# Optimization experiments

Measured on AMD Instinct MI355X. Metric: run time of the kernel, lower is better.

The kernel has to match this reference:

```python
import jax, jax.numpy as jnp
import numpy as np

N_HEAD = 12
D_MODEL = 768
B, T = 1, 1024


def _rope(x):
    # x: (B, H, T, Dh). Matches torch RoPE: split even/odd, cat halves.
    Dh = x.shape[-1]
    t = x.shape[2]
    inv_freq = 1.0 / (10000.0 ** (jnp.arange(0, Dh, 2, dtype=jnp.float32) / Dh))
    freqs = jnp.arange(t, dtype=jnp.float32)[:, None] * inv_freq[None, :]  # (T, Dh/2)
    cos = jnp.cos(freqs)[None, None]  # (1,1,T,Dh/2)
    sin = jnp.sin(freqs)[None, None]
    x1 = x[..., 0::2]
    x2 = x[..., 1::2]
    return jnp.concatenate([-x2 * sin + x1 * cos, x1 * sin + x2 * cos], axis=-1)


def _wedge(x, A, id_bias):
    # S = (A - A^T) + diag(id_bias_h), per head h; x: (B,H,T,Dh)
    skew = A - A.T  # (Dh, Dh)
    S = skew[None, :, :] + jax.vmap(jnp.diag)(id_bias)  # (H, Dh, Dh)
    flow = jnp.einsum('bhtd,hde->bhte', x, S)
    return x + flow


def _forward(x, WV_w, WV_b, WK_w, WK_b, WQ_w, A, id_bias, sink, v_nulls, WO_w, WO_b):
    b, t, c = x.shape
    n_br = WO_w.shape[0]
    n_sh = n_br
    dh = c // n_br
    h_tot = n_br * n_sh
    scale = dh ** -0.5

    q = (x @ WQ_w).reshape(b, t, h_tot, dh).transpose(0, 2, 1, 3)      # (B,Htot,T,Dh)
    k_base = (x @ WK_w + WK_b).reshape(b, t, n_sh, dh).transpose(0, 2, 1, 3)
    v_base = (x @ WV_w + WV_b).reshape(b, t, n_sh, dh).transpose(0, 2, 1, 3)
    k = jnp.tile(k_base, (1, n_br, 1, 1))  # (B,Htot,T,Dh)
    v = jnp.tile(v_base, (1, n_br, 1, 1))

    q = _rope(_wedge(q, A, id_bias))
    k = _rope(_wedge(k, A, id_bias))

    scores = jnp.einsum('bhtd,bhsd->bhts', q, k) * scale  # (B,Htot,T,T)
    causal = jnp.tril(jnp.ones((t, t), dtype=bool))
    scores = jnp.where(causal[None, None], scores, -jnp.inf)

    sinks = jnp.broadcast_to(sink.reshape(1, h_tot, 1, 1), (b, h_tot, t, 1))
    probs = jax.nn.softmax(jnp.concatenate([scores, sinks], axis=-1), axis=-1)
    probs_tok, probs_sink = probs[..., :t], probs[..., t:]

    out_tok = jnp.einsum('bhts,bhsd->bhtd', probs_tok, v)
    out_sink = probs_sink * v_nulls.reshape(h_tot, dh)[None, :, None, :]
    ctx = out_tok + out_sink  # (B,Htot,T,Dh)

    ctx = ctx.reshape(b, n_br, n_sh, t, dh).transpose(0, 1, 3, 2, 4).reshape(b, n_br, t, c)
    y = jnp.einsum('bntc,ncd->bntd', ctx, WO_w) + WO_b[None, :, None, :]
    return y.mean(axis=1)  # (B,T,C)


def setup_inputs() -> dict:
    key = jax.random.key(0)
    ks = jax.random.split(key, 12)
    c = D_MODEL
    n_br = N_HEAD
    dh = c // n_br
    h_tot = n_br * n_br
    s = 0.02
    return {
        'x': jax.random.normal(ks[0], (B, T, c), dtype=jnp.float32),
        'WV_w': jax.random.normal(ks[1], (c, c), dtype=jnp.float32) * s,
        'WV_b': jnp.zeros((c,), dtype=jnp.float32),
        'WK_w': jax.random.normal(ks[2], (c, c), dtype=jnp.float32) * s,
        'WK_b': jnp.zeros((c,), dtype=jnp.float32),
        'WQ_w': jax.random.normal(ks[3], (c, c * n_br), dtype=jnp.float32) * s,
        'A': jax.random.normal(ks[4], (dh, dh), dtype=jnp.float32) * s,
        'id_bias': jax.random.normal(ks[5], (h_tot, dh), dtype=jnp.float32) * s,
        'sink': jax.random.normal(ks[6], (h_tot,), dtype=jnp.float32) * s,
        'v_nulls': jax.random.normal(ks[7], (n_br, c), dtype=jnp.float32) * s,
        'WO_w': jax.random.normal(ks[8], (n_br, c, c), dtype=jnp.float32) * (1.0 / np.sqrt(c)),
        'WO_b': jnp.zeros((n_br, c), dtype=jnp.float32),
    }


def reference(x, WV_w, WV_b, WK_w, WK_b, WQ_w, A, id_bias, sink, v_nulls, WO_w, WO_b):
    return _forward(x, WV_w, WV_b, WK_w, WK_b, WQ_w, A, id_bias, sink, v_nulls, WO_w, WO_b)
```

## Files before the change

kernel.cpp:

```cpp
#include <hip/hip_runtime.h>
#include <hip/hip_bf16.h>

#define T_SEQ   1024
#define C_MODEL 768
#define N_BR    12
#define DH      64
#define H_TOT   144
#define NQ      9216

typedef __bf16 bf16x8 __attribute__((ext_vector_type(8)));
typedef float  f32x4  __attribute__((ext_vector_type(4)));
typedef unsigned short u16;

#define SM_OFF 3.0f

__device__ __forceinline__ void gload16(void* lds, const void* g)
{
    __builtin_amdgcn_global_load_lds(
        (const __attribute__((address_space(1))) void*)g,
        (__attribute__((address_space(3))) void*)lds, 16, 0, 0);
}

__device__ __forceinline__ void split1(float x, u16& h, u16& l)
{
    __bf16 bh = (__bf16)x;
    __bf16 bl = (__bf16)(x - (float)bh);
    h = __builtin_bit_cast(u16, bh);
    l = __builtin_bit_cast(u16, bl);
}

__device__ __forceinline__ u16 tobf(float x)
{
    return __builtin_bit_cast(u16, (__bf16)x);
}

__device__ __forceinline__ int swb(int row, int byteoff)
{
    return row * 128 + (byteoff ^ ((row & 7) << 4));
}

__device__ __forceinline__ bf16x8 ldsr8(const u16* p, int byteoff)
{
    return *reinterpret_cast<const bf16x8*>(reinterpret_cast<const char*>(p) + byteoff);
}

__device__ __forceinline__ void convt_body(const float* __restrict__ W,
                                           u16* __restrict__ out, int K, int N,
                                           int nx, int ky, float (*t)[33], int tid)
{
    const int n0 = nx * 32;
    const int k0 = ky * 32;
    const int tx = tid & 31;
    const int ty = tid >> 5;
    #pragma unroll
    for (int r = 0; r < 4; ++r)
        t[ty + r * 8][tx] = W[(size_t)(k0 + ty + r * 8) * N + n0 + tx];
    __syncthreads();
    #pragma unroll
    for (int r = 0; r < 4; ++r)
        out[(size_t)(n0 + ty + r * 8) * K + k0 + tx] = tobf(t[tx][ty + r * 8]);
}

__global__ __launch_bounds__(256)
void prep_kernel(const float* __restrict__ x, u16* __restrict__ xh,
                 const float* __restrict__ Amat, const float* __restrict__ id_bias,
                 u16* __restrict__ Mth, u16* __restrict__ Mtl,
                 const float* __restrict__ WO_b, float* __restrict__ mbias,
                 float* __restrict__ tab,
                 const float* __restrict__ WO_w, u16* __restrict__ wot,
                 const float* __restrict__ WK_w, const float* __restrict__ WV_w,
                 u16* __restrict__ wkvt)
{
    __shared__ float tsh[32][33];
    const int b   = blockIdx.x;
    const int tid = threadIdx.x;

    if (b < 128) {
        const int idx = b * 256 + tid;
        const int t = idx >> 5, i = idx & 31;
        const float inv = expf(-(float)i * (logf(10000.f) / 32.f));
        const float fr = (float)t * inv;
        tab[t * 64 + i]      = cosf(fr);
        tab[t * 64 + 32 + i] = sinf(fr);
    } else if (b < 272) {
        const int h = b - 128;
        const int base = tid * 16;
        #pragma unroll
        for (int i = 0; i < 16; ++i) {
            const int idx = base + i;
            const int e = idx >> 6, d = idx & 63;
            float v = Amat[d * 64 + e] - Amat[e * 64 + d];
            if (d == e) v += 1.0f + id_bias[h * 64 + d];
            u16 hh, ll;
            split1(v, hh, ll);
            Mth[(size_t)h * 4096 + idx] = hh;
            Mtl[(size_t)h * 4096 + idx] = ll;
        }
    } else if (b < 275) {
        const int d = (b - 272) * 256 + tid;
        if (d < C_MODEL) {
            float s = 0.f;
            #pragma unroll
            for (int n = 0; n < N_BR; ++n) s += WO_b[n * C_MODEL + d];
            mbias[d] = s * (1.0f / 12.0f);
        }
    } else if (b < 1043) {
        const size_t i = (size_t)(b - 275) * 1024 + tid * 4;
        float4 v = *reinterpret_cast<const float4*>(&x[i]);
        ushort4 o = { tobf(v.x), tobf(v.y), tobf(v.z), tobf(v.w) };
        *reinterpret_cast<ushort4*>(&xh[i]) = o;
    } else if (b < 7955) {
        const int u = b - 1043;
        convt_body(WO_w, wot, NQ, C_MODEL, u % 24, u / 24, tsh, tid);
    } else if (b < 8531) {
        const int u = b - 7955;
        convt_body(WK_w, wkvt, C_MODEL, C_MODEL, u % 24, u / 24, tsh, tid);
    } else {
        const int u = b - 8531;
        convt_body(WV_w, wkvt + 589824, C_MODEL, C_MODEL, u % 24, u / 24, tsh, tid);
    }
}

#define BM 128
#define BN 128
#define BK 32

__global__ __launch_bounds__(256)
void gemm_bf16_kernel(const u16* __restrict__ A, const u16* __restrict__ B,
                      float* __restrict__ Cp, int M, int N, int K)
{
    __shared__ __align__(16) u16 sA[BM * BK], sB[BN * BK];

    const int tid  = threadIdx.x;
    const int lane = tid & 63;
    const int wid  = tid >> 6;
    const int m0   = blockIdx.y * BM;
    const int n0   = blockIdx.x * BN;
    const int kc   = K / gridDim.z;
    const int kbeg = blockIdx.z * kc;
    const int kend = kbeg + kc;

    const int wm = (wid >> 1) * 64;
    const int wn = (wid & 1) * 64;

    f32x4 acc[4][4];
    #pragma unroll
    for (int i = 0; i < 4; ++i)
        #pragma unroll
        for (int j = 0; j < 4; ++j)
            #pragma unroll
            for (int r = 0; r < 4; ++r) acc[i][j][r] = 0.f;

    const int r0 = tid >> 2;
    const int c0 = tid & 3;
    const int rA = wm + (lane & 15);
    const int rB = wn + (lane & 15);
    const int co = (lane >> 4) * 8;

    for (int k0 = kbeg; k0 < kend; k0 += BK) {
        gload16(&sA[(size_t)tid * 8],         &A[(size_t)(m0 + r0)      * K + k0 + c0 * 8]);
        gload16(&sA[(size_t)(tid + 256) * 8], &A[(size_t)(m0 + r0 + 64) * K + k0 + c0 * 8]);
        gload16(&sB[(size_t)tid * 8],         &B[(size_t)(n0 + r0)      * K + k0 + c0 * 8]);
        gload16(&sB[(size_t)(tid + 256) * 8], &B[(size_t)(n0 + r0 + 64) * K + k0 + c0 * 8]);
        __syncthreads();

        bf16x8 ah[4], bh[4];
        #pragma unroll
        for (int i = 0; i < 4; ++i)
            ah[i] = *reinterpret_cast<const bf16x8*>(&sA[(size_t)(rA + i * 16) * BK + co]);
        #pragma unroll
        for (int j = 0; j < 4; ++j)
            bh[j] = *reinterpret_cast<const bf16x8*>(&sB[(size_t)(rB + j * 16) * BK + co]);
        #pragma unroll
        for (int i = 0; i < 4; ++i)
            #pragma unroll
            for (int j = 0; j < 4; ++j)
                acc[i][j] = __builtin_amdgcn_mfma_f32_16x16x32_bf16(ah[i], bh[j], acc[i][j], 0, 0, 0);
        __syncthreads();
    }

    float* Cz = Cp + (size_t)blockIdx.z * M * N;
    const int crow0 = m0 + wm + (lane >> 4) * 4;
    const int ccol0 = n0 + wn + (lane & 15);
    #pragma unroll
    for (int i = 0; i < 4; ++i)
        #pragma unroll
        for (int j = 0; j < 4; ++j)
            #pragma unroll
            for (int r = 0; r < 4; ++r)
                Cz[(size_t)(crow0 + i * 16 + r) * N + ccol0 + j * 16] = acc[i][j][r];
}

__global__ __launch_bounds__(256)
void gemm_q_rope_kernel(const u16* __restrict__ A, const u16* __restrict__ B,
                        const float* __restrict__ tab, u16* __restrict__ Q2)
{
    __shared__ __align__(16) u16 sA[BM * BK], sB[BN * BK];

    const int K = C_MODEL;
    const int tid  = threadIdx.x;
    const int lane = tid & 63;
    const int wid  = tid >> 6;
    const int m0   = blockIdx.y * BM;
    const int n0   = blockIdx.x * BN;

    const int wm = (wid >> 1) * 64;
    const int wn = (wid & 1) * 64;
    const int g  = lane >> 4;
    const int li = lane & 15;

    f32x4 acc[4][4];
    #pragma unroll
    for (int i = 0; i < 4; ++i)
        #pragma unroll
        for (int j = 0; j < 4; ++j)
            #pragma unroll
            for (int r = 0; r < 4; ++r) acc[i][j][r] = 0.f;

    const int r0 = tid >> 2;
    const int c0 = tid & 3;
    const int rA = wm + li;
    const int rB = wn + li;
    const int co = g * 8;

    for (int k0 = 0; k0 < K; k0 += BK) {
        gload16(&sA[(size_t)tid * 8],         &A[(size_t)(m0 + r0)      * K + k0 + c0 * 8]);
        gload16(&sA[(size_t)(tid + 256) * 8], &A[(size_t)(m0 + r0 + 64) * K + k0 + c0 * 8]);
        gload16(&sB[(size_t)tid * 8],         &B[(size_t)(n0 + r0)      * K + k0 + c0 * 8]);
        gload16(&sB[(size_t)(tid + 256) * 8], &B[(size_t)(n0 + r0 + 64) * K + k0 + c0 * 8]);
        __syncthreads();

        bf16x8 ah[4], bh[4];
        #pragma unroll
        for (int i = 0; i < 4; ++i)
            ah[i] = *reinterpret_cast<const bf16x8*>(&sA[(size_t)(rA + i * 16) * BK + co]);
        #pragma unroll
        for (int j = 0; j < 4; ++j)
            bh[j] = *reinterpret_cast<const bf16x8*>(&sB[(size_t)(rB + j * 16) * BK + co]);
        #pragma unroll
        for (int i = 0; i < 4; ++i)
            #pragma unroll
            for (int j = 0; j < 4; ++j)
                acc[i][j] = __builtin_amdgcn_mfma_f32_16x16x32_bf16(ah[i], bh[j], acc[i][j], 0, 0, 0);
        __syncthreads();
    }

    const int h  = (n0 + wn) >> 6;
    const bool ev = (li & 1) == 0;
    #pragma unroll
    for (int j = 0; j < 4; ++j) {
        const int e  = j * 16 + li;
        const int i2 = e >> 1;
        #pragma unroll
        for (int i = 0; i < 4; ++i) {
            #pragma unroll
            for (int r = 0; r < 4; ++r) {
                const int t = m0 + wm + i * 16 + g * 4 + r;
                const float own = acc[i][j][r];
                const float oth = __shfl_xor(own, 1);
                const float cs = tab[t * 64 + i2];
                const float sn = tab[t * 64 + 32 + i2];
                float o; int ch;
                if (ev) { o = own * cs - oth * sn; ch = i2; }
                else    { o = oth * sn + own * cs; ch = 32 + i2; }
                Q2[((size_t)h * T_SEQ + t) * 64 + ch] = tobf(o * 0.125f);
            }
        }
    }
}

__global__ __launch_bounds__(256)
void reduce_kernel(const float* __restrict__ part, float* __restrict__ out,
                   const float* __restrict__ bias, int MN, int N, int Z, float alpha)
{
    const int i = (blockIdx.x * 256 + threadIdx.x) * 4;
    if (i >= MN) return;
    float4 s = *reinterpret_cast<const float4*>(&part[i]);
    for (int z = 1; z < Z; ++z) {
        float4 p = *reinterpret_cast<const float4*>(&part[(size_t)z * MN + i]);
        s.x += p.x; s.y += p.y; s.z += p.z; s.w += p.w;
    }
    s.x *= alpha; s.y *= alpha; s.z *= alpha; s.w *= alpha;
    if (bias) {
        const int c = i % N;
        s.x += bias[c]; s.y += bias[c + 1]; s.z += bias[c + 2]; s.w += bias[c + 3];
    }
    *reinterpret_cast<float4*>(&out[i]) = s;
}

__global__ __launch_bounds__(256)
void reduce_kv_kernel(const float* __restrict__ part, float* __restrict__ out,
                      const float* __restrict__ kb, const float* __restrict__ vb,
                      int MN, int Z)
{
    const int i = (blockIdx.x * 256 + threadIdx.x) * 4;
    if (i >= MN) return;
    float4 s = *reinterpret_cast<const float4*>(&part[i]);
    for (int z = 1; z < Z; ++z) {
        float4 p = *reinterpret_cast<const float4*>(&part[(size_t)z * MN + i]);
        s.x += p.x; s.y += p.y; s.z += p.z; s.w += p.w;
    }
    const int c = i % 1536;
    const float* bp = (c < 768) ? (kb + c) : (vb + c - 768);
    s.x += bp[0]; s.y += bp[1]; s.z += bp[2]; s.w += bp[3];
    *reinterpret_cast<float4*>(&out[i]) = s;
}

__global__ __launch_bounds__(256)
void fold_wq_kernel(const float* __restrict__ WQ, const u16* __restrict__ Mth,
                    const u16* __restrict__ Mtl, u16* __restrict__ wqt)
{
    __shared__ __align__(16) u16 sMh[4096], sMl[4096];
    __shared__ __align__(16) u16 sB[8192];

    const int h   = blockIdx.x;
    const int k0  = blockIdx.y * 128;
    const int tid = threadIdx.x;
    const int lane = tid & 63, w = tid >> 6, g = lane >> 4, li = lane & 15;

    {
        const char* gmh = (const char*)(Mth + (size_t)h * 4096);
        const char* gml = (const char*)(Mtl + (size_t)h * 4096);
        #pragma unroll
        for (int p = 0; p < 2; ++p) {
            const int u = p * 256 + tid;
            const int row = u >> 3, off = (u & 7) * 16;
            const int src = swb(row, off);
            gload16((char*)sMh + u * 16, gmh + src);
            gload16((char*)sMl + u * 16, gml + src);
        }
    }
    {
        const int r    = tid >> 1;
        const int half = tid & 1;
        const float* src = WQ + (size_t)(k0 + r) * NQ + h * 64 + half * 32;
        #pragma unroll
        for (int q = 0; q < 8; ++q) {
            float4 v = *reinterpret_cast<const float4*>(&src[q * 4]);
            ushort4 o = { tobf(v.x), tobf(v.y), tobf(v.z), tobf(v.w) };
            const int byte = swb(r, half * 64 + q * 8);
            *reinterpret_cast<ushort4*>(reinterpret_cast<char*>(sB) + byte) = o;
        }
    }
    __syncthreads();

    f32x4 acc[4][2];
    #pragma unroll
    for (int i = 0; i < 4; ++i)
        #pragma unroll
        for (int jj = 0; jj < 2; ++jj)
            #pragma unroll
            for (int r = 0; r < 4; ++r) acc[i][jj][r] = 0.f;

    bf16x8 ah[4][2], al[4][2];
    #pragma unroll
    for (int i = 0; i < 4; ++i)
        #pragma unroll
        for (int ks = 0; ks < 2; ++ks) {
            ah[i][ks] = ldsr8(sMh, swb(16 * i + li, ks * 64 + g * 16));
            al[i][ks] = ldsr8(sMl, swb(16 * i + li, ks * 64 + g * 16));
        }
    #pragma unroll
    for (int jj = 0; jj < 2; ++jj) {
        const int brow = 16 * (2 * w + jj) + li;
        #pragma unroll
        for (int ks = 0; ks < 2; ++ks) {
            bf16x8 bh = ldsr8(sB, swb(brow, ks * 64 + g * 16));
            #pragma unroll
            for (int i = 0; i < 4; ++i) {
                acc[i][jj] = __builtin_amdgcn_mfma_f32_16x16x32_bf16(ah[i][ks], bh, acc[i][jj], 0, 0, 0);
                acc[i][jj] = __builtin_amdgcn_mfma_f32_16x16x32_bf16(al[i][ks], bh, acc[i][jj], 0, 0, 0);
            }
        }
    }

    #pragma unroll
    for (int i = 0; i < 4; ++i)
        #pragma unroll
        for (int jj = 0; jj < 2; ++jj) {
            const int kc = k0 + 16 * (2 * w + jj) + li;
            #pragma unroll
            for (int r = 0; r < 4; ++r) {
                const int e = 16 * i + g * 4 + r;
                wqt[((size_t)h * 64 + e) * 768 + kc] = tobf(acc[i][jj][r]);
            }
        }
}

__global__ __launch_bounds__(256)
void wedge_mfma_kernel(const float* __restrict__ X, u16* __restrict__ Y,
                       const u16* __restrict__ Mth, const u16* __restrict__ Mtl,
                       const float* __restrict__ tab, int inStride, int headMod)
{
    const int h   = blockIdx.x;
    const int t0  = blockIdx.y * 64;
    const int tid = threadIdx.x;
    const int lane = tid & 63;
    const int w    = tid >> 6;
    const int g    = lane >> 4;
    const int li   = lane & 15;

    __shared__ __align__(16) u16 sX[4096], sMh[4096], sMl[4096];

    {
        const int r  = tid >> 2;
        const int c0 = (tid & 3) * 16;
        const float* xrow = X + (size_t)(t0 + r) * inStride + (h % headMod) * 64;
        #pragma unroll
        for (int q = 0; q < 4; ++q) {
            const int c = c0 + q * 4;
            float4 v = *reinterpret_cast<const float4*>(&xrow[c]);
            ushort4 hv = { tobf(v.x), tobf(v.y), tobf(v.z), tobf(v.w) };
            *reinterpret_cast<ushort4*>(reinterpret_cast<char*>(sX) + swb(r, 2 * c)) = hv;
        }
    }
    {
        const char* gmh = (const char*)(Mth + (size_t)h * 4096);
        const char* gml = (const char*)(Mtl + (size_t)h * 4096);
        #pragma unroll
        for (int u = 0; u < 2; ++u) {
            const int L = (u * 256 + tid) * 16;
            const int row = L >> 7, off = L & 127;
            const int src = swb(row, off);
            gload16(reinterpret_cast<char*>(sMh) + L, gmh + src);
            gload16(reinterpret_cast<char*>(sMl) + L, gml + src);
        }
    }
    __syncthreads();

    f32x4 acc[4];
    #pragma unroll
    for (int j = 0; j < 4; ++j)
        #pragma unroll
        for (int r = 0; r < 4; ++r) acc[j][r] = 0.f;

    bf16x8 ah[2];
    #pragma unroll
    for (int ks = 0; ks < 2; ++ks)
        ah[ks] = ldsr8(sX, swb(w * 16 + li, ks * 64 + g * 16));
    #pragma unroll
    for (int ks = 0; ks < 2; ++ks)
        #pragma unroll
        for (int j = 0; j < 4; ++j) {
            bf16x8 bh = ldsr8(sMh, swb(16 * j + li, ks * 64 + g * 16));
            bf16x8 bl = ldsr8(sMl, swb(16 * j + li, ks * 64 + g * 16));
            acc[j] = __builtin_amdgcn_mfma_f32_16x16x32_bf16(ah[ks], bh, acc[j], 0, 0, 0);
            acc[j] = __builtin_amdgcn_mfma_f32_16x16x32_bf16(ah[ks], bl, acc[j], 0, 0, 0);
        }

    const bool ev = (li & 1) == 0;
    #pragma unroll
    for (int j = 0; j < 4; ++j) {
        const int e = 16 * j + li;
        const int i2 = e >> 1;
        #pragma unroll
        for (int r = 0; r < 4; ++r) {
            const int t = t0 + w * 16 + g * 4 + r;
            const float own = acc[j][r];
            const float oth = __shfl_xor(own, 1);
            const float cs = tab[t * 64 + i2];
            const float sn = tab[t * 64 + 32 + i2];
            float o; int ch;
            if (ev) { o = own * cs - oth * sn; ch = i2; }
            else    { o = oth * sn + own * cs; ch = 32 + i2; }
            Y[((size_t)h * T_SEQ + t) * 64 + ch] = tobf(o);
        }
    }
}

__global__ __launch_bounds__(256)
void vt_kernel(const float* __restrict__ vb, u16* __restrict__ Vt, int stride)
{
    __shared__ float Ls[64][65];
    const int s  = blockIdx.x;
    const int t0 = blockIdx.y * 64;
    const int tid = threadIdx.x;
    {
        const int r  = tid >> 2;
        const int c0 = (tid & 3) * 16;
        const float* row = vb + (size_t)(t0 + r) * stride + s * 64;
        #pragma unroll
        for (int q = 0; q < 4; ++q) {
            float4 v = *reinterpret_cast<const float4*>(&row[c0 + q * 4]);
            Ls[r][c0 + q * 4 + 0] = v.x; Ls[r][c0 + q * 4 + 1] = v.y;
            Ls[r][c0 + q * 4 + 2] = v.z; Ls[r][c0 + q * 4 + 3] = v.w;
        }
    }
    __syncthreads();
    {
        const int d  = tid >> 2;
        const int tq = (tid & 3) * 16;
        u16* orow = Vt + ((size_t)s * 64 + d) * T_SEQ + t0 + tq;
        #pragma unroll
        for (int q = 0; q < 4; ++q) {
            ushort4 o;
            o.x = tobf(Ls[tq + q * 4 + 0][d]);
            o.y = tobf(Ls[tq + q * 4 + 1][d]);
            o.z = tobf(Ls[tq + q * 4 + 2][d]);
            o.w = tobf(Ls[tq + q * 4 + 3][d]);
            *reinterpret_cast<ushort4*>(&orow[q * 4]) = o;
        }
    }
}

template<bool DIAG>
__device__ __forceinline__ void attn_tile64(
    int kv0, int rowb, int h, int s, int tid, int w, int g, int li,
    const u16* __restrict__ K2, const u16* __restrict__ Vt,
    u16* sK, u16* sV, u16* sP, const bf16x8* qa,
    f32x4* acc, float* psum)
{
    {
        const char* gk = (const char*)(K2 + ((size_t)h * T_SEQ + kv0) * 64);
        const char* gv = (const char*)Vt + (size_t)s * 131072 + kv0 * 2;
        #pragma unroll
        for (int p = 0; p < 2; ++p) {
            const int u = p * 256 + tid;
            const int row = u >> 3, off = (u & 7) * 16;
            gload16((char*)sK + u * 16, gk + row * 128 + (off ^ ((row & 7) << 4)));
            gload16((char*)sV + u * 16, gv + row * 2048 + (off ^ ((row & 7) << 4)));
        }
    }
    __syncthreads();

    f32x4 sacc[4];
    #pragma unroll
    for (int j = 0; j < 4; ++j)
        #pragma unroll
        for (int r = 0; r < 4; ++r) sacc[j][r] = 0.f;

    __builtin_amdgcn_s_setprio(1);
    #pragma unroll
    for (int ks = 0; ks < 2; ++ks)
        #pragma unroll
        for (int j = 0; j < 4; ++j) {
            bf16x8 kb = ldsr8(sK, swb(16 * j + li, ks * 64 + g * 16));
            sacc[j] = __builtin_amdgcn_mfma_f32_16x16x32_bf16(qa[ks], kb, sacc[j], 0, 0, 0);
        }
    __builtin_amdgcn_s_setprio(0);

    char* pb = (char*)sP + w * 2048;
    #pragma unroll
    for (int j = 0; j < 4; ++j) {
        const int colj = kv0 + 16 * j + li;
        #pragma unroll
        for (int r = 0; r < 4; ++r) {
            float sv_ = sacc[j][r];
            if (DIAG && colj > rowb + r) sv_ = -__builtin_inff();
            const float p = __expf(sv_ - SM_OFF);
            psum[r] += p;
            const int prow = g * 4 + r;
            *reinterpret_cast<u16*>(pb + prow * 128 +
                ((2 * (16 * j + li)) ^ ((prow & 7) << 4))) = tobf(p);
        }
    }

    __builtin_amdgcn_s_setprio(1);
    #pragma unroll
    for (int ks = 0; ks < 2; ++ks) {
        bf16x8 pa = *reinterpret_cast<const bf16x8*>(
            pb + li * 128 + ((ks * 64 + g * 16) ^ ((li & 7) << 4)));
        #pragma unroll
        for (int j = 0; j < 4; ++j) {
            bf16x8 vb = ldsr8(sV, swb(16 * j + li, ks * 64 + g * 16));
            acc[j] = __builtin_amdgcn_mfma_f32_16x16x32_bf16(pa, vb, acc[j], 0, 0, 0);
        }
    }
    __builtin_amdgcn_s_setprio(0);
    __syncthreads();
}

__global__ __launch_bounds__(256)
void attn_mfma_kernel(const u16* __restrict__ Q2, const u16* __restrict__ K2,
                      const u16* __restrict__ Vt, const float* __restrict__ sink,
                      const float* __restrict__ v_nulls, u16* __restrict__ ctxb)
{
    const int h  = blockIdx.x;
    const int qt = 15 - (int)blockIdx.y;
    const int s  = h % N_BR;
    const int tid  = threadIdx.x;
    const int lane = tid & 63, w = tid >> 6, g = lane >> 4, li = lane & 15;

    __shared__ __align__(16) u16 sQ[4096];
    __shared__ __align__(16) u16 sK[4096];
    __shared__ __align__(16) u16 sV[4096];
    __shared__ __align__(16) u16 sP[4096];

    {
        const char* gq = (const char*)(Q2 + ((size_t)h * T_SEQ + qt * 64) * 64);
        #pragma unroll
        for (int p = 0; p < 2; ++p) {
            const int u = p * 256 + tid;
            const int row = u >> 3, off = (u & 7) * 16;
            gload16((char*)sQ + u * 16, gq + row * 128 + (off ^ ((row & 7) << 4)));
        }
    }
    __syncthreads();

    bf16x8 qa[2];
    #pragma unroll
    for (int ks = 0; ks < 2; ++ks)
        qa[ks] = ldsr8(sQ, swb(w * 16 + li, ks * 64 + g * 16));

    f32x4 acc[4];
    #pragma unroll
    for (int j = 0; j < 4; ++j)
        #pragma unroll
        for (int r = 0; r < 4; ++r) acc[j][r] = 0.f;
    float psum[4] = {0.f, 0.f, 0.f, 0.f};

    const int rowb = qt * 64 + w * 16 + g * 4;
    for (int kt = 0; kt < qt; ++kt)
        attn_tile64<false>(kt * 64, rowb, h, s, tid, w, g, li, K2, Vt, sK, sV, sP, qa, acc, psum);
    attn_tile64<true>(qt * 64, rowb, h, s, tid, w, g, li, K2, Vt, sK, sV, sP, qa, acc, psum);

    #pragma unroll
    for (int r = 0; r < 4; ++r)
        #pragma unroll
        for (int d = 8; d >= 1; d >>= 1) psum[r] += __shfl_xor(psum[r], d);

    const float es = __expf(sink[h] - SM_OFF);
    #pragma unroll
    for (int r = 0; r < 4; ++r) {
        const float rz = 1.0f / (psum[r] + es);
        const int trow = qt * 64 + w * 16 + g * 4 + r;
        #pragma unroll
        for (int j = 0; j < 4; ++j) {
            const int col = 16 * j + li;
            const float outv = (acc[j][r] + es * v_nulls[h * 64 + col]) * rz;
            ctxb[(size_t)trow * NQ + h * 64 + col] = tobf(outv);
        }
    }
}

extern "C" void kernel_launch(void* const* d_in, const int* in_sizes, int n_in,
                              void* d_out, int out_size, void* d_ws, size_t ws_size,
                              hipStream_t stream)
{
    (void)in_sizes; (void)n_in; (void)out_size; (void)ws_size;

    const float* x       = (const float*)d_in[0];
    const float* WV_w    = (const float*)d_in[1];
    const float* WV_b    = (const float*)d_in[2];
    const float* WK_w    = (const float*)d_in[3];
    const float* WK_b    = (const float*)d_in[4];
    const float* WQ_w    = (const float*)d_in[5];
    const float* Amat    = (const float*)d_in[6];
    const float* id_bias = (const float*)d_in[7];
    const float* sink    = (const float*)d_in[8];
    const float* v_nulls = (const float*)d_in[9];
    const float* WO_w    = (const float*)d_in[10];
    const float* WO_b    = (const float*)d_in[11];
    float* out = (float*)d_out;

    float* tab    = (float*)d_ws;
    float* mbias  = tab + 65536;
    float* kvbase = mbias + 768;
    u16* Mth  = (u16*)(kvbase + 1572864);
    u16* Mtl  = Mth + 589824;
    u16* xh   = Mtl + 589824;
    u16* wqt  = xh + 786432;
    u16* wkvt = wqt + 7077888;
    u16* wot  = wkvt + 1179648;
    u16* K2   = wot + 7077888;
    u16* Vt   = K2 + 9437184;
    u16* Q2   = Vt + 786432;
    u16* ctxb = Q2 + 9437184;
    float* pkv = (float*)(ctxb + 9437184);

    float* outpart = (float*)K2;

    const dim3 blk(256);

    prep_kernel<<<dim3(9107), blk, 0, stream>>>(
        x, xh, Amat, id_bias, Mth, Mtl, WO_b, mbias, tab, WO_w, wot, WK_w, WV_w, wkvt);

    fold_wq_kernel<<<dim3(H_TOT, 6), blk, 0, stream>>>(WQ_w, Mth, Mtl, wqt);

    gemm_bf16_kernel<<<dim3(12, 8, 4), blk, 0, stream>>>(
        xh, wkvt, pkv, T_SEQ, 1536, C_MODEL);
    reduce_kv_kernel<<<dim3(1536), blk, 0, stream>>>(pkv, kvbase, WK_b, WV_b, 1572864, 4);

    wedge_mfma_kernel<<<dim3(H_TOT, 16), blk, 0, stream>>>(
        kvbase, K2, Mth, Mtl, tab, 1536, N_BR);
    vt_kernel<<<dim3(12, 16), blk, 0, stream>>>(kvbase + 768, Vt, 1536);

    gemm_q_rope_kernel<<<dim3(72, 8), blk, 0, stream>>>(xh, wqt, tab, Q2);

    attn_mfma_kernel<<<dim3(H_TOT, 16), blk, 0, stream>>>(
        Q2, K2, Vt, sink, v_nulls, ctxb);

    gemm_bf16_kernel<<<dim3(6, 8, 12), blk, 0, stream>>>(
        ctxb, wot, outpart, T_SEQ, C_MODEL, NQ);
    reduce_kernel<<<dim3(768), blk, 0, stream>>>(
        outpart, out, mbias, 786432, C_MODEL, 12, 1.0f / 12.0f);
}
```

Before: 191.4 us.

## Double-buffer attention K/V, keep P in registers, shrink GEMM M-tiles

The attention kernel now double-buffers K/V tiles in LDS, prefetching the next tile while computing the current one. It swaps MFMA operand order so the S^T layout lets the probabilities be packed straight into bf16 registers, which removes the shared-memory P round trip and one barrier per tile. The Q-projection and output GEMMs move to 64x128 tiles with twice as many blocks, aiming for better occupancy and wave count. In exchange, LDS use and the index logic grow, and the K rows are permuted on load to match the transposed layout.

```diff
diff --git a/kernel.cpp b/kernel.cpp
--- a/kernel.cpp
+++ b/kernel.cpp
@@ -10,6 +10,7 @@
 
 typedef __bf16 bf16x8 __attribute__((ext_vector_type(8)));
 typedef float  f32x4  __attribute__((ext_vector_type(4)));
+typedef unsigned int u32x4 __attribute__((ext_vector_type(4)));
 typedef unsigned short u16;
 
 #define SM_OFF 3.0f
@@ -32,6 +33,13 @@
 __device__ __forceinline__ u16 tobf(float x)
 {
     return __builtin_bit_cast(u16, (__bf16)x);
+}
+
+__device__ __forceinline__ unsigned cvtpk(float a, float b)
+{
+    unsigned r;
+    asm("v_cvt_pk_bf16_f32 %0, %1, %2" : "=v"(r) : "v"(a), "v"(b));
+    return r;
 }
 
 __device__ __forceinline__ int swb(int row, int byteoff)
@@ -192,53 +200,113 @@
 }
 
 __global__ __launch_bounds__(256)
+void gemm64_kernel(const u16* __restrict__ A, const u16* __restrict__ B,
+                   float* __restrict__ Cp, int M, int N, int K)
+{
+    __shared__ __align__(16) u16 sA[64 * BK], sB[128 * BK];
+
+    const int tid  = threadIdx.x;
+    const int lane = tid & 63;
+    const int wid  = tid >> 6;
+    const int m0   = blockIdx.y * 64;
+    const int n0   = blockIdx.x * 128;
+    const int kc   = K / gridDim.z;
+    const int kbeg = blockIdx.z * kc;
+    const int kend = kbeg + kc;
+
+    const int wm = (wid >> 1) * 32;
+    const int wn = (wid & 1) * 64;
+    const int g  = lane >> 4;
+    const int li = lane & 15;
+
+    f32x4 acc[2][4];
+    #pragma unroll
+    for (int i = 0; i < 2; ++i)
+        #pragma unroll
+        for (int j = 0; j < 4; ++j)
+            #pragma unroll
+            for (int r = 0; r < 4; ++r) acc[i][j][r] = 0.f;
+
+    const int r0 = tid >> 2;
+    const int c0 = (tid & 3) * 8;
+
+    for (int k0 = kbeg; k0 < kend; k0 += BK) {
+        gload16(&sA[(size_t)tid * 8],         &A[(size_t)(m0 + r0)      * K + k0 + c0]);
+        gload16(&sB[(size_t)tid * 8],         &B[(size_t)(n0 + r0)      * K + k0 + c0]);
+        gload16(&sB[(size_t)(tid + 256) * 8], &B[(size_t)(n0 + r0 + 64) * K + k0 + c0]);
+        __syncthreads();
+
+        bf16x8 ah[2], bh[4];
+        #pragma unroll
+        for (int i = 0; i < 2; ++i)
+            ah[i] = *reinterpret_cast<const bf16x8*>(&sA[(size_t)(wm + 16 * i + li) * BK + g * 8]);
+        #pragma unroll
+        for (int j = 0; j < 4; ++j)
+            bh[j] = *reinterpret_cast<const bf16x8*>(&sB[(size_t)(wn + 16 * j + li) * BK + g * 8]);
+        #pragma unroll
+        for (int i = 0; i < 2; ++i)
+            #pragma unroll
+            for (int j = 0; j < 4; ++j)
+                acc[i][j] = __builtin_amdgcn_mfma_f32_16x16x32_bf16(ah[i], bh[j], acc[i][j], 0, 0, 0);
+        __syncthreads();
+    }
+
+    float* Cz = Cp + (size_t)blockIdx.z * M * N;
+    const int crow0 = m0 + wm + g * 4;
+    const int ccol0 = n0 + wn + li;
+    #pragma unroll
+    for (int i = 0; i < 2; ++i)
+        #pragma unroll
+        for (int j = 0; j < 4; ++j)
+            #pragma unroll
+            for (int r = 0; r < 4; ++r)
+                Cz[(size_t)(crow0 + i * 16 + r) * N + ccol0 + j * 16] = acc[i][j][r];
+}
+
+__global__ __launch_bounds__(256)
 void gemm_q_rope_kernel(const u16* __restrict__ A, const u16* __restrict__ B,
                         const float* __restrict__ tab, u16* __restrict__ Q2)
 {
-    __shared__ __align__(16) u16 sA[BM * BK], sB[BN * BK];
+    __shared__ __align__(16) u16 sA[64 * BK], sB[128 * BK];
 
     const int K = C_MODEL;
     const int tid  = threadIdx.x;
     const int lane = tid & 63;
     const int wid  = tid >> 6;
-    const int m0   = blockIdx.y * BM;
-    const int n0   = blockIdx.x * BN;
-
-    const int wm = (wid >> 1) * 64;
+    const int m0   = blockIdx.y * 64;
+    const int n0   = blockIdx.x * 128;
+
+    const int wm = (wid >> 1) * 32;
     const int wn = (wid & 1) * 64;
     const int g  = lane >> 4;
     const int li = lane & 15;
 
-    f32x4 acc[4][4];
-    #pragma unroll
-    for (int i = 0; i < 4; ++i)
+    f32x4 acc[2][4];
+    #pragma unroll
+    for (int i = 0; i < 2; ++i)
         #pragma unroll
         for (int j = 0; j < 4; ++j)
             #pragma unroll
             for (int r = 0; r < 4; ++r) acc[i][j][r] = 0.f;
 
     const int r0 = tid >> 2;
-    const int c0 = tid & 3;
-    const int rA = wm + li;
-    const int rB = wn + li;
-    const int co = g * 8;
+    const int c0 = (tid & 3) * 8;
 
     for (int k0 = 0; k0 < K; k0 += BK) {
-        gload16(&sA[(size_t)tid * 8],         &A[(size_t)(m0 + r0)      * K + k0 + c0 * 8]);
-        gload16(&sA[(size_t)(tid + 256) * 8], &A[(size_t)(m0 + r0 + 64) * K + k0 + c0 * 8]);
-        gload16(&sB[(size_t)tid * 8],         &B[(size_t)(n0 + r0)      * K + k0 + c0 * 8]);
-        gload16(&sB[(size_t)(tid + 256) * 8], &B[(size_t)(n0 + r0 + 64) * K + k0 + c0 * 8]);
+        gload16(&sA[(size_t)tid * 8],         &A[(size_t)(m0 + r0)      * K + k0 + c0]);
+        gload16(&sB[(size_t)tid * 8],         &B[(size_t)(n0 + r0)      * K + k0 + c0]);
+        gload16(&sB[(size_t)(tid + 256) * 8], &B[(size_t)(n0 + r0 + 64) * K + k0 + c0]);
         __syncthreads();
 
-        bf16x8 ah[4], bh[4];
-        #pragma unroll
-        for (int i = 0; i < 4; ++i)
-            ah[i] = *reinterpret_cast<const bf16x8*>(&sA[(size_t)(rA + i * 16) * BK + co]);
+        bf16x8 ah[2], bh[4];
+        #pragma unroll
+        for (int i = 0; i < 2; ++i)
+            ah[i] = *reinterpret_cast<const bf16x8*>(&sA[(size_t)(wm + 16 * i + li) * BK + g * 8]);
         #pragma unroll
         for (int j = 0; j < 4; ++j)
-            bh[j] = *reinterpret_cast<const bf16x8*>(&sB[(size_t)(rB + j * 16) * BK + co]);
-        #pragma unroll
-        for (int i = 0; i < 4; ++i)
+            bh[j] = *reinterpret_cast<const bf16x8*>(&sB[(size_t)(wn + 16 * j + li) * BK + g * 8]);
+        #pragma unroll
+        for (int i = 0; i < 2; ++i)
             #pragma unroll
             for (int j = 0; j < 4; ++j)
                 acc[i][j] = __builtin_amdgcn_mfma_f32_16x16x32_bf16(ah[i], bh[j], acc[i][j], 0, 0, 0);
@@ -252,7 +320,7 @@
         const int e  = j * 16 + li;
         const int i2 = e >> 1;
         #pragma unroll
-        for (int i = 0; i < 4; ++i) {
+        for (int i = 0; i < 2; ++i) {
             #pragma unroll
             for (int r = 0; r < 4; ++r) {
                 const int t = m0 + wm + i * 16 + g * 4 + r;
@@ -503,26 +571,32 @@
     }
 }
 
+__device__ __forceinline__ void attn_stage_kv(
+    int buf, int kv0, int h, int s, int tid,
+    const u16* __restrict__ K2, const u16* __restrict__ Vt,
+    u16* sK, u16* sV)
+{
+    const char* gk = (const char*)(K2 + ((size_t)h * T_SEQ + kv0) * 64);
+    const char* gv = (const char*)Vt + (size_t)s * 131072 + kv0 * 2;
+    #pragma unroll
+    for (int p = 0; p < 2; ++p) {
+        const int u = p * 256 + tid;
+        const int row = u >> 3;
+        const int off = (u & 7) * 16;
+        const int sw  = off ^ ((row & 7) << 4);
+        const int j  = row >> 4, g2 = (row >> 2) & 3, rr = row & 3;
+        const int srow = 32 * (j & 1) + 8 * g2 + 4 * (j >> 1) + rr;
+        gload16((char*)sK + buf * 8192 + u * 16, gk + srow * 128 + sw);
+        gload16((char*)sV + buf * 8192 + u * 16, gv + row * 2048 + sw);
+    }
+}
+
 template<bool DIAG>
-__device__ __forceinline__ void attn_tile64(
-    int kv0, int rowb, int h, int s, int tid, int w, int g, int li,
-    const u16* __restrict__ K2, const u16* __restrict__ Vt,
-    u16* sK, u16* sV, u16* sP, const bf16x8* qa,
-    f32x4* acc, float* psum)
-{
-    {
-        const char* gk = (const char*)(K2 + ((size_t)h * T_SEQ + kv0) * 64);
-        const char* gv = (const char*)Vt + (size_t)s * 131072 + kv0 * 2;
-        #pragma unroll
-        for (int p = 0; p < 2; ++p) {
-            const int u = p * 256 + tid;
-            const int row = u >> 3, off = (u & 7) * 16;
-            gload16((char*)sK + u * 16, gk + row * 128 + (off ^ ((row & 7) << 4)));
-            gload16((char*)sV + u * 16, gv + row * 2048 + (off ^ ((row & 7) << 4)));
-        }
-    }
-    __syncthreads();
-
+__device__ __forceinline__ void attn_tile_sw(
+    int kv0, int qglob, int g, int li,
+    const u16* sK, const u16* sV, const bf16x8* qa,
+    f32x4* acc, float& psum)
+{
     f32x4 sacc[4];
     #pragma unroll
     for (int j = 0; j < 4; ++j)
@@ -535,39 +609,44 @@
         #pragma unroll
         for (int j = 0; j < 4; ++j) {
             bf16x8 kb = ldsr8(sK, swb(16 * j + li, ks * 64 + g * 16));
-            sacc[j] = __builtin_amdgcn_mfma_f32_16x16x32_bf16(qa[ks], kb, sacc[j], 0, 0, 0);
+            sacc[j] = __builtin_amdgcn_mfma_f32_16x16x32_bf16(kb, qa[ks], sacc[j], 0, 0, 0);
         }
     __builtin_amdgcn_s_setprio(0);
 
-    char* pb = (char*)sP + w * 2048;
-    #pragma unroll
-    for (int j = 0; j < 4; ++j) {
-        const int colj = kv0 + 16 * j + li;
+    float p[4][4];
+    const int kvb = kv0 + 8 * g;
+    #pragma unroll
+    for (int j = 0; j < 4; ++j)
         #pragma unroll
         for (int r = 0; r < 4; ++r) {
             float sv_ = sacc[j][r];
-            if (DIAG && colj > rowb + r) sv_ = -__builtin_inff();
-            const float p = __expf(sv_ - SM_OFF);
-            psum[r] += p;
-            const int prow = g * 4 + r;
-            *reinterpret_cast<u16*>(pb + prow * 128 +
-                ((2 * (16 * j + li)) ^ ((prow & 7) << 4))) = tobf(p);
-        }
-    }
+            if (DIAG) {
+                const int kv = kvb + 32 * (j & 1) + 4 * (j >> 1) + r;
+                if (kv > qglob) sv_ = -__builtin_inff();
+            }
+            p[j][r] = __expf(sv_ - SM_OFF);
+        }
+    psum += ((p[0][0] + p[0][1]) + (p[0][2] + p[0][3]))
+          + ((p[1][0] + p[1][1]) + (p[1][2] + p[1][3]))
+          + ((p[2][0] + p[2][1]) + (p[2][2] + p[2][3]))
+          + ((p[3][0] + p[3][1]) + (p[3][2] + p[3][3]));
 
     __builtin_amdgcn_s_setprio(1);
     #pragma unroll
     for (int ks = 0; ks < 2; ++ks) {
-        bf16x8 pa = *reinterpret_cast<const bf16x8*>(
-            pb + li * 128 + ((ks * 64 + g * 16) ^ ((li & 7) << 4)));
+        u32x4 pw;
+        pw[0] = cvtpk(p[ks][0],     p[ks][1]);
+        pw[1] = cvtpk(p[ks][2],     p[ks][3]);
+        pw[2] = cvtpk(p[ks + 2][0], p[ks + 2][1]);
+        pw[3] = cvtpk(p[ks + 2][2], p[ks + 2][3]);
+        bf16x8 pa = __builtin_bit_cast(bf16x8, pw);
         #pragma unroll
         for (int j = 0; j < 4; ++j) {
             bf16x8 vb = ldsr8(sV, swb(16 * j + li, ks * 64 + g * 16));
-            acc[j] = __builtin_amdgcn_mfma_f32_16x16x32_bf16(pa, vb, acc[j], 0, 0, 0);
+            acc[j] = __builtin_amdgcn_mfma_f32_16x16x32_bf16(vb, pa, acc[j], 0, 0, 0);
         }
     }
     __builtin_amdgcn_s_setprio(0);
-    __syncthreads();
 }
 
 __global__ __launch_bounds__(256)
@@ -582,9 +661,8 @@
     const int lane = tid & 63, w = tid >> 6, g = lane >> 4, li = lane & 15;
 
     __shared__ __align__(16) u16 sQ[4096];
-    __shared__ __align__(16) u16 sK[4096];
-    __shared__ __align__(16) u16 sV[4096];
-    __shared__ __align__(16) u16 sP[4096];
+    __shared__ __align__(16) u16 sK[8192];
+    __shared__ __align__(16) u16 sV[8192];
 
     {
         const char* gq = (const char*)(Q2 + ((size_t)h * T_SEQ + qt * 64) * 64);
@@ -595,6 +673,7 @@
             gload16((char*)sQ + u * 16, gq + row * 128 + (off ^ ((row & 7) << 4)));
         }
     }
+    attn_stage_kv(0, 0, h, s, tid, K2, Vt, sK, sV);
     __syncthreads();
 
     bf16x8 qa[2];
@@ -607,29 +686,39 @@
     for (int j = 0; j < 4; ++j)
         #pragma unroll
         for (int r = 0; r < 4; ++r) acc[j][r] = 0.f;
-    float psum[4] = {0.f, 0.f, 0.f, 0.f};
-
-    const int rowb = qt * 64 + w * 16 + g * 4;
-    for (int kt = 0; kt < qt; ++kt)
-        attn_tile64<false>(kt * 64, rowb, h, s, tid, w, g, li, K2, Vt, sK, sV, sP, qa, acc, psum);
-    attn_tile64<true>(qt * 64, rowb, h, s, tid, w, g, li, K2, Vt, sK, sV, sP, qa, acc, psum);
-
-    #pragma unroll
-    for (int r = 0; r < 4; ++r)
-        #pragma unroll
-        for (int d = 8; d >= 1; d >>= 1) psum[r] += __shfl_xor(psum[r], d);
-
+    float psum = 0.f;
+
+    const int qglob = qt * 64 + w * 16 + li;
+    const int nt = qt + 1;
+    int cur = 0;
+    for (int kt = 0; kt < nt - 1; ++kt) {
+        attn_stage_kv(cur ^ 1, (kt + 1) * 64, h, s, tid, K2, Vt, sK, sV);
+        attn_tile_sw<false>(kt * 64, qglob, g, li,
+                            sK + cur * 4096, sV + cur * 4096, qa, acc, psum);
+        __syncthreads();
+        cur ^= 1;
+    }
+    attn_tile_sw<true>(qt * 64, qglob, g, li,
+                       sK + cur * 4096, sV + cur * 4096, qa, acc, psum);
+
+    psum += __shfl_xor(psum, 16);
+    psum += __shfl_xor(psum, 32);
     const float es = __expf(sink[h] - SM_OFF);
-    #pragma unroll
-    for (int r = 0; r < 4; ++r) {
-        const float rz = 1.0f / (psum[r] + es);
-        const int trow = qt * 64 + w * 16 + g * 4 + r;
-        #pragma unroll
-        for (int j = 0; j < 4; ++j) {
-            const int col = 16 * j + li;
-            const float outv = (acc[j][r] + es * v_nulls[h * 64 + col]) * rz;
-            ctxb[(size_t)trow * NQ + h * 64 + col] = tobf(outv);
-        }
+    const float rz = 1.0f / (psum + es);
+
+    const int t = qt * 64 + w * 16 + li;
+    u16* orow = ctxb + (size_t)t * NQ + h * 64;
+    const float* vn = v_nulls + h * 64;
+    #pragma unroll
+    for (int j = 0; j < 4; ++j) {
+        const int d0 = 16 * j + 4 * g;
+        float4 vnv = *reinterpret_cast<const float4*>(&vn[d0]);
+        ushort4 o;
+        o.x = tobf((acc[j][0] + es * vnv.x) * rz);
+        o.y = tobf((acc[j][1] + es * vnv.y) * rz);
+        o.z = tobf((acc[j][2] + es * vnv.z) * rz);
+        o.w = tobf((acc[j][3] + es * vnv.w) * rz);
+        *reinterpret_cast<ushort4*>(&orow[d0]) = o;
     }
 }
 
@@ -685,12 +774,12 @@
         kvbase, K2, Mth, Mtl, tab, 1536, N_BR);
     vt_kernel<<<dim3(12, 16), blk, 0, stream>>>(kvbase + 768, Vt, 1536);
 
-    gemm_q_rope_kernel<<<dim3(72, 8), blk, 0, stream>>>(xh, wqt, tab, Q2);
+    gemm_q_rope_kernel<<<dim3(72, 16), blk, 0, stream>>>(xh, wqt, tab, Q2);
 
     attn_mfma_kernel<<<dim3(H_TOT, 16), blk, 0, stream>>>(
         Q2, K2, Vt, sink, v_nulls, ctxb);
 
-    gemm_bf16_kernel<<<dim3(6, 8, 12), blk, 0, stream>>>(
+    gemm64_kernel<<<dim3(6, 16, 12), blk, 0, stream>>>(
         ctxb, wot, outpart, T_SEQ, C_MODEL, NQ);
     reduce_kernel<<<dim3(768), blk, 0, stream>>>(
         outpart, out, mbias, 786432, C_MODEL, 12, 1.0f / 12.0f);
```

After: 181.2 us. 5.3% less time.
